# Kernel optimization log

Measured on AMD Instinct MI355X. Metric: run time of the kernel, lower is better.

## Reference

```python
import jax, jax.numpy as jnp
import numpy as np

N = 1024
D_X = 128
D_Y = 128
NUM_STEPS = 200


def setup_inputs() -> dict:
    key = jax.random.key(0)
    k1, k2, k3, k4, k5 = jax.random.split(key, 5)
    init_samples_x = jax.random.normal(k1, (N, D_X), dtype=jnp.float32)
    init_samples_y = jax.random.normal(k2, (N, D_Y), dtype=jnp.float32)
    mean_final = jax.random.normal(k3, (D_X,), dtype=jnp.float32)
    # variance must be positive and bounded away from zero
    var_final = jax.random.uniform(k4, (D_X,), dtype=jnp.float32, minval=0.25, maxval=0.75)
    gammas = jnp.linspace(1e-3, 1e-2, NUM_STEPS, dtype=jnp.float32)
    # pre-generated per-step Gaussian noise (replaces torch.randn inside the loop)
    noise = jax.random.normal(k5, (NUM_STEPS, N, D_X), dtype=jnp.float32)
    return {
        "init_samples_x": init_samples_x,
        "init_samples_y": init_samples_y,
        "mean_final": mean_final,
        "var_final": var_final,
        "gammas": gammas,
        "noise": noise,
    }


def reference(init_samples_x, init_samples_y, mean_final, var_final, gammas, noise):
    """Faithful JAX port of Langevin.record_init_langevin.

    grad_gauss(x, m, v) = -(x - m) / v
    per step k:
        t_old = x + gamma_k * grad_gauss(x)
        x     = t_old + sqrt(2*gamma_k) * z_k
        t_new = x + gamma_k * grad_gauss(x)
        record x, y, t_old - t_new
    """
    num_steps = gammas.shape[0]
    n = init_samples_x.shape[0]

    def step(x, inp):
        gamma, z = inp
        t_old = x + gamma * (-(x - mean_final) / var_final)
        x_new = t_old + jnp.sqrt(2.0 * gamma) * z
        t_new = x_new + gamma * (-(x_new - mean_final) / var_final)
        return x_new, (x_new, t_old - t_new)

    _, (xs, outs) = jax.lax.scan(step, init_samples_x, (gammas, noise))
    # scan stacks along leading (step) axis -> [S, N, D]; match torch layout [N, S, D]
    x_tot = jnp.transpose(xs, (1, 0, 2))
    out = jnp.transpose(outs, (1, 0, 2))
    # y is constant across steps; the torch loop just replicates it
    y_tot = jnp.broadcast_to(init_samples_y[:, None, :], (n, num_steps, init_samples_y.shape[1]))
    steps_expanded = jnp.broadcast_to(
        jnp.arange(num_steps, dtype=jnp.int32)[None, :, None], (n, num_steps, 1)
    )
    return x_tot, y_tot, out, steps_expanded
```

## Files before the change

kernel.cpp:

```cpp
#include <hip/hip_runtime.h>
#include <math.h>

constexpr int N  = 1024;
constexpr int D  = 128;
constexpr int S  = 200;
constexpr int D2 = D / 2;

__global__ __launch_bounds__(256, 4) void langevin_kernel(
    const float2* __restrict__ x0,
    const float2* __restrict__ y0,
    const float2* __restrict__ mean,
    const float2* __restrict__ var,
    const float*  __restrict__ gammas,
    const float2* __restrict__ noise,
    float2* __restrict__ x_tot,
    float2* __restrict__ y_tot,
    float2* __restrict__ outp,
    float*  __restrict__ steps)
{
    __shared__ float sg[S];
    __shared__ float ss[S];
    for (int i = threadIdx.x; i < S; i += 256) {
        float g = gammas[i];
        sg[i] = g;
        ss[i] = sqrtf(2.0f * g);
    }
    __syncthreads();

    const int idx = blockIdx.x * 256 + threadIdx.x;
    const int n   = idx >> 6;
    const int dp  = idx & 63;

    float2 x       = x0[idx];
    const float2 y = y0[idx];
    const float2 m = mean[dp];
    const float2 v = var[dp];
    const float ivx = 1.0f / v.x;
    const float ivy = 1.0f / v.y;

    const float2* zp = noise + idx;
    float2* xq = x_tot + (size_t)n * (S * D2) + dp;
    float2* yq = y_tot + (size_t)n * (S * D2) + dp;
    float2* oq = outp  + (size_t)n * (S * D2) + dp;
    float*  sq = steps + (size_t)n * S;

    #pragma unroll 4
    for (int k = 0; k < S; ++k) {
        const float g = sg[k];
        const float s = ss[k];
        const float2 z = zp[(size_t)k * (N * D2)];

        const float gx = g * ivx;
        const float gy = g * ivy;

        const float tox = fmaf(-gx, x.x - m.x, x.x);
        const float toy = fmaf(-gy, x.y - m.y, x.y);
        x.x = fmaf(s, z.x, tox);
        x.y = fmaf(s, z.y, toy);
        const float tnx = fmaf(-gx, x.x - m.x, x.x);
        const float tny = fmaf(-gy, x.y - m.y, x.y);

        float2 o;
        o.x = tox - tnx;
        o.y = toy - tny;

        xq[(size_t)k * D2] = x;
        yq[(size_t)k * D2] = y;
        oq[(size_t)k * D2] = o;
        if (dp == 0) sq[k] = (float)k;
    }
}

extern "C" void kernel_launch(void* const* d_in, const int* in_sizes, int n_in,
                              void* d_out, int out_size, void* d_ws, size_t ws_size,
                              hipStream_t stream)
{
    const float* x0     = (const float*)d_in[0];
    const float* y0     = (const float*)d_in[1];
    const float* mean   = (const float*)d_in[2];
    const float* var    = (const float*)d_in[3];
    const float* gammas = (const float*)d_in[4];
    const float* noise  = (const float*)d_in[5];

    float* x_tot = (float*)d_out;
    float* y_tot = x_tot + (size_t)N * S * D;
    float* outp  = y_tot + (size_t)N * S * D;
    float* steps = outp  + (size_t)N * S * D;

    dim3 grid((N * D2) / 256);
    dim3 block(256);
    langevin_kernel<<<grid, block, 0, stream>>>(
        (const float2*)x0, (const float2*)y0, (const float2*)mean,
        (const float2*)var, gammas, (const float2*)noise,
        (float2*)x_tot, (float2*)y_tot, (float2*)outp, steps);
}
```

Measured before the change: 475.2 us.

## Switch to scalar per-thread elements with nontemporal loads and stores

```diff
diff --git a/kernel.cpp b/kernel.cpp
--- a/kernel.cpp
+++ b/kernel.cpp
@@ -1,22 +1,21 @@
 #include <hip/hip_runtime.h>
 #include <math.h>
 
-constexpr int N  = 1024;
-constexpr int D  = 128;
-constexpr int S  = 200;
-constexpr int D2 = D / 2;
+constexpr int N = 1024;
+constexpr int D = 128;
+constexpr int S = 200;
 
-__global__ __launch_bounds__(256, 4) void langevin_kernel(
-    const float2* __restrict__ x0,
-    const float2* __restrict__ y0,
-    const float2* __restrict__ mean,
-    const float2* __restrict__ var,
-    const float*  __restrict__ gammas,
-    const float2* __restrict__ noise,
-    float2* __restrict__ x_tot,
-    float2* __restrict__ y_tot,
-    float2* __restrict__ outp,
-    float*  __restrict__ steps)
+__global__ __launch_bounds__(256, 2) void langevin_kernel(
+    const float* __restrict__ x0,
+    const float* __restrict__ y0,
+    const float* __restrict__ mean,
+    const float* __restrict__ var,
+    const float* __restrict__ gammas,
+    const float* __restrict__ noise,
+    float* __restrict__ x_tot,
+    float* __restrict__ y_tot,
+    float* __restrict__ outp,
+    float* __restrict__ steps)
 {
     __shared__ float sg[S];
     __shared__ float ss[S];
@@ -28,46 +27,37 @@
     __syncthreads();
 
     const int idx = blockIdx.x * 256 + threadIdx.x;
-    const int n   = idx >> 6;
-    const int dp  = idx & 63;
+    const int n   = idx >> 7;
+    const int d   = idx & (D - 1);
 
-    float2 x       = x0[idx];
-    const float2 y = y0[idx];
-    const float2 m = mean[dp];
-    const float2 v = var[dp];
-    const float ivx = 1.0f / v.x;
-    const float ivy = 1.0f / v.y;
+    float x       = x0[idx];
+    const float y = y0[idx];
+    const float m = mean[d];
+    const float iv = 1.0f / var[d];
 
-    const float2* zp = noise + idx;
-    float2* xq = x_tot + (size_t)n * (S * D2) + dp;
-    float2* yq = y_tot + (size_t)n * (S * D2) + dp;
-    float2* oq = outp  + (size_t)n * (S * D2) + dp;
-    float*  sq = steps + (size_t)n * S;
+    const float* zp = noise + idx;
+    const size_t base = (size_t)n * (S * D) + d;
+    float* xq = x_tot + base;
+    float* yq = y_tot + base;
+    float* oq = outp  + base;
+    float* sq = steps + (size_t)n * S;
 
-    #pragma unroll 4
+    #pragma unroll 8
     for (int k = 0; k < S; ++k) {
         const float g = sg[k];
         const float s = ss[k];
-        const float2 z = zp[(size_t)k * (N * D2)];
+        const float z = __builtin_nontemporal_load(zp + (size_t)k * (N * D));
 
-        const float gx = g * ivx;
-        const float gy = g * ivy;
+        const float gv = g * iv;
+        const float to = fmaf(-gv, x - m, x);
+        x = fmaf(s, z, to);
+        const float tn = fmaf(-gv, x - m, x);
+        const float o  = to - tn;
 
-        const float tox = fmaf(-gx, x.x - m.x, x.x);
-        const float toy = fmaf(-gy, x.y - m.y, x.y);
-        x.x = fmaf(s, z.x, tox);
-        x.y = fmaf(s, z.y, toy);
-        const float tnx = fmaf(-gx, x.x - m.x, x.x);
-        const float tny = fmaf(-gy, x.y - m.y, x.y);
-
-        float2 o;
-        o.x = tox - tnx;
-        o.y = toy - tny;
-
-        xq[(size_t)k * D2] = x;
-        yq[(size_t)k * D2] = y;
-        oq[(size_t)k * D2] = o;
-        if (dp == 0) sq[k] = (float)k;
+        __builtin_nontemporal_store(x, xq + (size_t)k * D);
+        __builtin_nontemporal_store(y, yq + (size_t)k * D);
+        __builtin_nontemporal_store(o, oq + (size_t)k * D);
+        if (d == 0) __builtin_nontemporal_store((float)k, sq + k);
     }
 }
 
@@ -87,10 +77,8 @@
     float* outp  = y_tot + (size_t)N * S * D;
     float* steps = outp  + (size_t)N * S * D;
 
-    dim3 grid((N * D2) / 256);
+    dim3 grid((N * D) / 256);
     dim3 block(256);
     langevin_kernel<<<grid, block, 0, stream>>>(
-        (const float2*)x0, (const float2*)y0, (const float2*)mean,
-        (const float2*)var, gammas, (const float2*)noise,
-        (float2*)x_tot, (float2*)y_tot, (float2*)outp, steps);
+        x0, y0, mean, var, gammas, noise, x_tot, y_tot, outp, steps);
 }
```

Result: no change. 477.4 us (+0.5%).
